# Kernel optimization log

Hardware: AMD Instinct MI355X
Metric: run time of the kernel (lower is better)

## Reference

```python
import jax, jax.numpy as jnp
import numpy as np

NUM_LEVELS = 8
CODEBOOK_SIZE = 1024
D_MODEL = 512


def setup_inputs() -> dict:
    key = jax.random.key(0)
    kx, kc = jax.random.split(key)
    x = jax.random.normal(kx, (8, 4096, D_MODEL), dtype=jnp.float32)
    # stacked embedding tables, one per RVQ level: [L, K, D]
    codebooks = jax.random.normal(kc, (NUM_LEVELS, CODEBOOK_SIZE, D_MODEL), dtype=jnp.float32)
    return {"x": x, "codebooks": codebooks}


def reference(x, codebooks):
    """Residual VQ: per level, nearest-codebook lookup on the residual.

    x: [B, N, D], codebooks: [L, K, D].
    Returns (quantized [B, N, D] with straight-through estimator, indices [B, N, L]).
    """
    residual = x
    q_sum = jnp.zeros_like(x)
    all_indices = []
    for l in range(codebooks.shape[0]):
        cb = codebooks[l]  # [K, D]
        # squared Euclidean distance; argmin matches torch.cdist argmin
        r2 = jnp.sum(residual * residual, axis=-1, keepdims=True)      # [B, N, 1]
        c2 = jnp.sum(cb * cb, axis=-1)                                  # [K]
        cross = jnp.einsum("bnd,kd->bnk", residual, cb)                # [B, N, K]
        dist2 = r2 - 2.0 * cross + c2                                   # [B, N, K]
        idx = jnp.argmin(dist2, axis=-1)                                # [B, N]
        all_indices.append(idx)
        q = cb[idx]                                                     # gather: [B, N, D]
        q_sum = q_sum + q
        residual = residual - q
    # straight-through: forward value is q_sum, gradient flows to x only
    quantized = x + jax.lax.stop_gradient(q_sum - x)
    return quantized, jnp.stack(all_indices, axis=-1)
```

## Files before the change

kernel.cpp:

```cpp
#include <hip/hip_runtime.h>
#include <stdint.h>

#define NLV 8
#define KCB 1024
#define DM  512
#define NTOK (8*4096)
#define BETA 0.00390625f

typedef _Float16 f16;
typedef f16  f16x4 __attribute__((ext_vector_type(4)));
typedef f16  f16x8 __attribute__((ext_vector_type(8)));
typedef float f32x4 __attribute__((ext_vector_type(4)));

typedef __attribute__((address_space(1))) const unsigned int* as1p;
typedef __attribute__((address_space(3))) unsigned int*       as3p;
__device__ __forceinline__ void gll16(const void* g, void* l) {
    __builtin_amdgcn_global_load_lds((as1p)g, (as3p)l, 16, 0, 0);
}

__global__ void c2_kernel(const float* __restrict__ cbs, float* __restrict__ c2) {
    int row  = blockIdx.x;
    int lane = threadIdx.x;
    const float4* p4 = (const float4*)(cbs + (size_t)row * DM);
    float4 a = p4[lane];
    float4 b = p4[lane + 64];
    float s = a.x*a.x + a.y*a.y + a.z*a.z + a.w*a.w
            + b.x*b.x + b.y*b.y + b.z*b.z + b.w*b.w;
    float t = (float)(f16)a.x + (float)(f16)a.y + (float)(f16)a.z + (float)(f16)a.w
            + (float)(f16)b.x + (float)(f16)b.y + (float)(f16)b.z + (float)(f16)b.w;
    #pragma unroll
    for (int off = 32; off > 0; off >>= 1) {
        s += __shfl_down(s, off, 64);
        t += __shfl_down(t, off, 64);
    }
    if (lane == 0) c2[row] = s + 2.0f * BETA * t;
}

__global__ void split_kernel(const float* __restrict__ src,
                             f16* __restrict__ hi, f16* __restrict__ lo) {
    size_t i = (size_t)blockIdx.x * 256 + threadIdx.x;
    float4 v = ((const float4*)src)[i];
    f16x4 h, l;
    h.x = (f16)v.x; l.x = (f16)((v.x - (float)h.x) + BETA);
    h.y = (f16)v.y; l.y = (f16)((v.y - (float)h.y) + BETA);
    h.z = (f16)v.z; l.z = (f16)((v.z - (float)h.z) + BETA);
    h.w = (f16)v.w; l.w = (f16)((v.w - (float)h.w) + BETA);
    ((f16x4*)hi)[i] = h;
    ((f16x4*)lo)[i] = l;
}

#define MBT  64
#define NCH  256
#define KS   32
#define NTHR 256
#define BUFB 40960

__global__ __launch_bounds__(NTHR, 2)
void rvq_mfma(const float* __restrict__ xin, float* __restrict__ qout,
              const float* __restrict__ cbs,
              const f16* __restrict__ Bhi, const f16* __restrict__ Blo,
              f16* __restrict__ Ahi, f16* __restrict__ Alo,
              const float* __restrict__ c2g, float* __restrict__ idxout,
              int lvl, int is_last)
{
    __shared__ char smem[2 * BUFB];
    const int tid  = threadIdx.x;
    const int lane = tid & 63;
    const int wn   = tid >> 6;
    const int tx   = lane & 15;
    const int q    = lane >> 4;
    const size_t tok0 = (size_t)blockIdx.x * MBT;

    const f16*   Bh_l = Bhi + (size_t)lvl * KCB * DM;
    const f16*   Bl_l = Blo + (size_t)lvl * KCB * DM;
    const float* c2l  = c2g + lvl * KCB;
    const float* cbl  = cbs + (size_t)lvl * KCB * DM;

    const int srow = tid >> 2;
    const int sg   = (tid & 3) ^ ((srow >> 1) & 3);
    const int rsw  = q ^ ((tx >> 1) & 3);

    auto stage = [&](char* buf, int cb0, int k0) {
        const int ko = k0 + sg * 8;
        char* wb = buf + wn * 1024;
        const size_t ga = (tok0 + srow) * (size_t)DM + ko;
        gll16(&Ahi[ga], wb);
        gll16(&Alo[ga], wb + 4096);
        #pragma unroll
        for (int i = 0; i < 4; ++i) {
            const size_t gb = (size_t)(cb0 + 64 * i + srow) * DM + ko;
            gll16(&Bh_l[gb], wb +  8192 + 4096 * i);
            gll16(&Bl_l[gb], wb + 24576 + 4096 * i);
        }
    };

    int aoff[4], boff[4];
    #pragma unroll
    for (int i = 0; i < 4; ++i) aoff[i] = (i * 16 + tx) * 64 + rsw * 16;
    #pragma unroll
    for (int j = 0; j < 4; ++j) boff[j] = (wn * 64 + j * 16 + tx) * 64 + rsw * 16;

    float bestv[16];
    int   besti[16];
    #pragma unroll
    for (int t = 0; t < 16; ++t) { bestv[t] = 3.4e38f; besti[t] = 0; }

    stage(smem, 0, 0);

    for (int ch = 0; ch < KCB / NCH; ++ch) {
        f32x4 acc[4][4];
        #pragma unroll
        for (int i = 0; i < 4; ++i)
            #pragma unroll
            for (int j = 0; j < 4; ++j) acc[i][j] = (f32x4)0.0f;

        for (int kk = 0; kk < 16; ++kk) {
            const int gk = ch * 16 + kk;
            char* bb = smem + (gk & 1) * BUFB;
            char* bn = smem + ((gk & 1) ^ 1) * BUFB;
            __syncthreads();
            if (gk + 1 < 64)
                stage(bn, ((gk + 1) >> 4) * NCH, ((gk + 1) & 15) * KS);

            f16x8 ah[4], al[4], bh[4], bl[4];
            #pragma unroll
            for (int i = 0; i < 4; ++i) {
                ah[i] = *(const f16x8*)(bb +        aoff[i]);
                al[i] = *(const f16x8*)(bb + 4096 + aoff[i]);
            }
            #pragma unroll
            for (int j = 0; j < 4; ++j) {
                bh[j] = *(const f16x8*)(bb +  8192 + boff[j]);
                bl[j] = *(const f16x8*)(bb + 24576 + boff[j]);
            }
            #pragma unroll
            for (int j = 0; j < 4; ++j)
                #pragma unroll
                for (int i = 0; i < 4; ++i)
                    acc[i][j] = __builtin_amdgcn_mfma_f32_16x16x32_f16(ah[i], bh[j], acc[i][j], 0, 0, 0);
            #pragma unroll
            for (int j = 0; j < 4; ++j)
                #pragma unroll
                for (int i = 0; i < 4; ++i)
                    acc[i][j] = __builtin_amdgcn_mfma_f32_16x16x32_f16(ah[i], bl[j], acc[i][j], 0, 0, 0);
            #pragma unroll
            for (int j = 0; j < 4; ++j)
                #pragma unroll
                for (int i = 0; i < 4; ++i)
                    acc[i][j] = __builtin_amdgcn_mfma_f32_16x16x32_f16(al[i], bh[j], acc[i][j], 0, 0, 0);
        }

        const int cb0 = ch * NCH;
        #pragma unroll
        for (int j = 0; j < 4; ++j) {
            int n = cb0 + wn * 64 + j * 16 + tx;
            float c2v = c2l[n];
            #pragma unroll
            for (int i = 0; i < 4; ++i)
                #pragma unroll
                for (int r = 0; r < 4; ++r) {
                    float s = fmaf(-2.f, acc[i][j][r], c2v);
                    int t = i * 4 + r;
                    if (s < bestv[t]) { bestv[t] = s; besti[t] = n; }
                }
        }
    }

    #pragma unroll
    for (int t = 0; t < 16; ++t) {
        float v = bestv[t]; int bi = besti[t];
        #pragma unroll
        for (int off = 1; off < 16; off <<= 1) {
            float ov = __shfl_xor(v, off, 64);
            int   oi = __shfl_xor(bi, off, 64);
            if (ov < v || (ov == v && oi < bi)) { v = ov; bi = oi; }
        }
        bestv[t] = v; besti[t] = bi;
    }

    float* redV = (float*)smem;
    int*   redI = (int*)(smem + 1024);
    int*   kbst = (int*)(smem + 2048);
    __syncthreads();
    if (tx == 0) {
        #pragma unroll
        for (int i = 0; i < 4; ++i)
            #pragma unroll
            for (int r = 0; r < 4; ++r) {
                int m = i * 16 + q * 4 + r;
                redV[wn * 64 + m] = bestv[i * 4 + r];
                redI[wn * 64 + m] = besti[i * 4 + r];
            }
    }
    __syncthreads();
    if (tid < MBT) {
        float bv = redV[tid]; int bi = redI[tid];
        #pragma unroll
        for (int w = 1; w < 4; ++w) {
            float v  = redV[w * 64 + tid];
            int   ii = redI[w * 64 + tid];
            if (v < bv || (v == bv && ii < bi)) { bv = v; bi = ii; }
        }
        kbst[tid] = bi;
        idxout[(tok0 + tid) * NLV + lvl] = (float)bi;
    }
    __syncthreads();

    #pragma unroll 4
    for (int it = 0; it < 16; ++it) {
        int e  = it * NTHR + tid;
        int t  = e >> 6, d8 = e & 63;
        size_t go = (tok0 + t) * (size_t)DM + d8 * 8;
        f16x8 h8 = *(const f16x8*)&Ahi[go];
        f16x8 l8 = *(const f16x8*)&Alo[go];
        const float* cp = &cbl[(size_t)kbst[t] * DM + d8 * 8];
        float4 c0 = *(const float4*)cp;
        float4 c1 = *(const float4*)(cp + 4);
        float r[8];
        r[0] = (float)h8[0] + ((float)l8[0] - BETA) - c0.x;
        r[1] = (float)h8[1] + ((float)l8[1] - BETA) - c0.y;
        r[2] = (float)h8[2] + ((float)l8[2] - BETA) - c0.z;
        r[3] = (float)h8[3] + ((float)l8[3] - BETA) - c0.w;
        r[4] = (float)h8[4] + ((float)l8[4] - BETA) - c1.x;
        r[5] = (float)h8[5] + ((float)l8[5] - BETA) - c1.y;
        r[6] = (float)h8[6] + ((float)l8[6] - BETA) - c1.z;
        r[7] = (float)h8[7] + ((float)l8[7] - BETA) - c1.w;
        if (is_last) {
            float4 x0 = *(const float4*)&xin[go];
            float4 x1 = *(const float4*)&xin[go + 4];
            float4 q0 = make_float4(x0.x - r[0], x0.y - r[1], x0.z - r[2], x0.w - r[3]);
            float4 q1 = make_float4(x1.x - r[4], x1.y - r[5], x1.z - r[6], x1.w - r[7]);
            *(float4*)&qout[go]     = q0;
            *(float4*)&qout[go + 4] = q1;
        } else {
            f16x8 h, l;
            #pragma unroll
            for (int k = 0; k < 8; ++k) {
                h[k] = (f16)r[k];
                l[k] = (f16)((r[k] - (float)h[k]) + BETA);
            }
            *(f16x8*)&Ahi[go] = h;
            *(f16x8*)&Alo[go] = l;
        }
    }
}

extern "C" void kernel_launch(void* const* d_in, const int* in_sizes, int n_in,
                              void* d_out, int out_size, void* d_ws, size_t ws_size,
                              hipStream_t stream) {
    const float* x   = (const float*)d_in[0];
    const float* cbs = (const float*)d_in[1];
    float* qout   = (float*)d_out;
    float* idxout = qout + (size_t)NTOK * DM;

    const size_t B_ELE = (size_t)NLV * KCB * DM;
    const size_t A_ELE = (size_t)NTOK * DM;

    f16* Bhi = (f16*)d_ws;
    f16* Blo = Bhi + B_ELE;
    f16* Ahi = Blo + B_ELE;
    f16* Alo = Ahi + A_ELE;
    float* c2 = (float*)(Alo + A_ELE);

    split_kernel<<<(int)(B_ELE / 4 / 256), 256, 0, stream>>>(cbs, Bhi, Blo);
    split_kernel<<<(int)(A_ELE / 4 / 256), 256, 0, stream>>>(x, Ahi, Alo);
    c2_kernel<<<NLV * KCB, 64, 0, stream>>>(cbs, c2);

    const int nblocks = NTOK / MBT;
    for (int l = 0; l < NLV; ++l) {
        rvq_mfma<<<nblocks, NTHR, 0, stream>>>(x, qout, cbs,
                                               Bhi, Blo, Ahi, Alo, c2, idxout,
                                               l, (l == NLV - 1) ? 1 : 0);
    }
}
```

Before: 1.131 ms.

## Load MFMA operands directly from global memory instead of LDS staging

Removes the double-buffered LDS staging (global_load_lds) and per-step barriers in the distance GEMM loop, and reads each wave's A/B fp16 hi/lo fragments directly from global memory. LDS shrinks to the small reduction buffers. This avoids barrier and staging overhead but makes every wave fetch A fragments redundantly through the caches, and removes explicit prefetch overlap, so load latency may be exposed.

```diff
diff --git a/kernel.cpp b/kernel.cpp
--- a/kernel.cpp
+++ b/kernel.cpp
@@ -11,12 +11,6 @@
 typedef f16  f16x4 __attribute__((ext_vector_type(4)));
 typedef f16  f16x8 __attribute__((ext_vector_type(8)));
 typedef float f32x4 __attribute__((ext_vector_type(4)));
-
-typedef __attribute__((address_space(1))) const unsigned int* as1p;
-typedef __attribute__((address_space(3))) unsigned int*       as3p;
-__device__ __forceinline__ void gll16(const void* g, void* l) {
-    __builtin_amdgcn_global_load_lds((as1p)g, (as3p)l, 16, 0, 0);
-}
 
 __global__ void c2_kernel(const float* __restrict__ cbs, float* __restrict__ c2) {
     int row  = blockIdx.x;
@@ -51,9 +45,7 @@
 
 #define MBT  64
 #define NCH  256
-#define KS   32
 #define NTHR 256
-#define BUFB 40960
 
 __global__ __launch_bounds__(NTHR, 2)
 void rvq_mfma(const float* __restrict__ xin, float* __restrict__ qout,
@@ -63,7 +55,10 @@
               const float* __restrict__ c2g, float* __restrict__ idxout,
               int lvl, int is_last)
 {
-    __shared__ char smem[2 * BUFB];
+    __shared__ float redV[4 * MBT];
+    __shared__ int   redI[4 * MBT];
+    __shared__ int   kbst[MBT];
+
     const int tid  = threadIdx.x;
     const int lane = tid & 63;
     const int wn   = tid >> 6;
@@ -71,68 +66,51 @@
     const int q    = lane >> 4;
     const size_t tok0 = (size_t)blockIdx.x * MBT;
 
-    const f16*   Bh_l = Bhi + (size_t)lvl * KCB * DM;
-    const f16*   Bl_l = Blo + (size_t)lvl * KCB * DM;
-    const float* c2l  = c2g + lvl * KCB;
-    const float* cbl  = cbs + (size_t)lvl * KCB * DM;
-
-    const int srow = tid >> 2;
-    const int sg   = (tid & 3) ^ ((srow >> 1) & 3);
-    const int rsw  = q ^ ((tx >> 1) & 3);
-
-    auto stage = [&](char* buf, int cb0, int k0) {
-        const int ko = k0 + sg * 8;
-        char* wb = buf + wn * 1024;
-        const size_t ga = (tok0 + srow) * (size_t)DM + ko;
-        gll16(&Ahi[ga], wb);
-        gll16(&Alo[ga], wb + 4096);
-        #pragma unroll
-        for (int i = 0; i < 4; ++i) {
-            const size_t gb = (size_t)(cb0 + 64 * i + srow) * DM + ko;
-            gll16(&Bh_l[gb], wb +  8192 + 4096 * i);
-            gll16(&Bl_l[gb], wb + 24576 + 4096 * i);
-        }
-    };
-
-    int aoff[4], boff[4];
-    #pragma unroll
-    for (int i = 0; i < 4; ++i) aoff[i] = (i * 16 + tx) * 64 + rsw * 16;
-    #pragma unroll
-    for (int j = 0; j < 4; ++j) boff[j] = (wn * 64 + j * 16 + tx) * 64 + rsw * 16;
+    const f16* __restrict__ Bh_l = Bhi + (size_t)lvl * KCB * DM;
+    const f16* __restrict__ Bl_l = Blo + (size_t)lvl * KCB * DM;
+    const float* __restrict__ c2l = c2g + lvl * KCB;
+    const float* __restrict__ cbl = cbs + (size_t)lvl * KCB * DM;
+
+    size_t abase[4];
+    #pragma unroll
+    for (int i = 0; i < 4; ++i)
+        abase[i] = (tok0 + (size_t)(i * 16 + tx)) * DM + q * 8;
 
     float bestv[16];
     int   besti[16];
     #pragma unroll
     for (int t = 0; t < 16; ++t) { bestv[t] = 3.4e38f; besti[t] = 0; }
 
-    stage(smem, 0, 0);
-
     for (int ch = 0; ch < KCB / NCH; ++ch) {
+        const int cb0 = ch * NCH;
+
+        size_t bbase[4];
+        #pragma unroll
+        for (int j = 0; j < 4; ++j)
+            bbase[j] = ((size_t)(cb0 + wn * 64 + j * 16 + tx)) * DM + q * 8;
+
         f32x4 acc[4][4];
         #pragma unroll
         for (int i = 0; i < 4; ++i)
             #pragma unroll
             for (int j = 0; j < 4; ++j) acc[i][j] = (f32x4)0.0f;
 
-        for (int kk = 0; kk < 16; ++kk) {
-            const int gk = ch * 16 + kk;
-            char* bb = smem + (gk & 1) * BUFB;
-            char* bn = smem + ((gk & 1) ^ 1) * BUFB;
-            __syncthreads();
-            if (gk + 1 < 64)
-                stage(bn, ((gk + 1) >> 4) * NCH, ((gk + 1) & 15) * KS);
+        #pragma unroll 4
+        for (int ks = 0; ks < 16; ++ks) {
+            const int ko = ks * 32;
 
             f16x8 ah[4], al[4], bh[4], bl[4];
             #pragma unroll
             for (int i = 0; i < 4; ++i) {
-                ah[i] = *(const f16x8*)(bb +        aoff[i]);
-                al[i] = *(const f16x8*)(bb + 4096 + aoff[i]);
+                ah[i] = *(const f16x8*)(Ahi + abase[i] + ko);
+                al[i] = *(const f16x8*)(Alo + abase[i] + ko);
             }
             #pragma unroll
             for (int j = 0; j < 4; ++j) {
-                bh[j] = *(const f16x8*)(bb +  8192 + boff[j]);
-                bl[j] = *(const f16x8*)(bb + 24576 + boff[j]);
-            }
+                bh[j] = *(const f16x8*)(Bh_l + bbase[j] + ko);
+                bl[j] = *(const f16x8*)(Bl_l + bbase[j] + ko);
+            }
+
             #pragma unroll
             for (int j = 0; j < 4; ++j)
                 #pragma unroll
@@ -150,7 +128,6 @@
                     acc[i][j] = __builtin_amdgcn_mfma_f32_16x16x32_f16(al[i], bh[j], acc[i][j], 0, 0, 0);
         }
 
-        const int cb0 = ch * NCH;
         #pragma unroll
         for (int j = 0; j < 4; ++j) {
             int n = cb0 + wn * 64 + j * 16 + tx;
@@ -178,10 +155,6 @@
         bestv[t] = v; besti[t] = bi;
     }
 
-    float* redV = (float*)smem;
-    int*   redI = (int*)(smem + 1024);
-    int*   kbst = (int*)(smem + 2048);
-    __syncthreads();
     if (tx == 0) {
         #pragma unroll
         for (int i = 0; i < 4; ++i)
```

Result: slower. 2.113 ms (+86.8%).

## Split operand staging into phases interleaved with MFMA groups and partial waits

Applied to the files above, without the earlier changes.

The single per-step stage-all-then-syncthreads pattern is replaced by three staged loads: A, then B-hi, then B-lo. Each is issued between MFMA groups and separated by raw s_barriers, with an explicit vmcnt wait instead of a full drain. MFMA sections are wrapped in s_setprio so compute waves get priority while the next tile streams in. The aim is to overlap global-to-LDS traffic with matrix math and cut full-barrier stalls. In exchange, stageA writes the next buffer before any barrier while slower waves may still be reading A-lo from that buffer, which risks a race. It also issues harmless extra loads on the final step.

```diff
diff --git a/kernel.cpp b/kernel.cpp
--- a/kernel.cpp
+++ b/kernel.cpp
@@ -17,6 +17,8 @@
 __device__ __forceinline__ void gll16(const void* g, void* l) {
     __builtin_amdgcn_global_load_lds((as1p)g, (as3p)l, 16, 0, 0);
 }
+
+#define VMCNT(n) asm volatile("s_waitcnt vmcnt(" #n ")" ::: "memory")
 
 __global__ void c2_kernel(const float* __restrict__ cbs, float* __restrict__ c2) {
     int row  = blockIdx.x;
@@ -80,18 +82,28 @@
     const int sg   = (tid & 3) ^ ((srow >> 1) & 3);
     const int rsw  = q ^ ((tx >> 1) & 3);
 
-    auto stage = [&](char* buf, int cb0, int k0) {
-        const int ko = k0 + sg * 8;
+    auto stageA = [&](char* buf, int gk2) {
+        const int ko = (gk2 & 15) * KS + sg * 8;
         char* wb = buf + wn * 1024;
         const size_t ga = (tok0 + srow) * (size_t)DM + ko;
         gll16(&Ahi[ga], wb);
         gll16(&Alo[ga], wb + 4096);
-        #pragma unroll
-        for (int i = 0; i < 4; ++i) {
-            const size_t gb = (size_t)(cb0 + 64 * i + srow) * DM + ko;
-            gll16(&Bh_l[gb], wb +  8192 + 4096 * i);
-            gll16(&Bl_l[gb], wb + 24576 + 4096 * i);
-        }
+    };
+    auto stageBh = [&](char* buf, int gk2) {
+        const int cb0 = (gk2 >> 4) * NCH;
+        const int ko  = (gk2 & 15) * KS + sg * 8;
+        char* wb = buf + wn * 1024;
+        #pragma unroll
+        for (int i = 0; i < 4; ++i)
+            gll16(&Bh_l[(size_t)(cb0 + 64 * i + srow) * DM + ko], wb + 8192 + 4096 * i);
+    };
+    auto stageBl = [&](char* buf, int gk2) {
+        const int cb0 = (gk2 >> 4) * NCH;
+        const int ko  = (gk2 & 15) * KS + sg * 8;
+        char* wb = buf + wn * 1024;
+        #pragma unroll
+        for (int i = 0; i < 4; ++i)
+            gll16(&Bl_l[(size_t)(cb0 + 64 * i + srow) * DM + ko], wb + 24576 + 4096 * i);
     };
 
     int aoff[4], boff[4];
@@ -105,7 +117,7 @@
     #pragma unroll
     for (int t = 0; t < 16; ++t) { bestv[t] = 3.4e38f; besti[t] = 0; }
 
-    stage(smem, 0, 0);
+    stageA(smem, 0); stageBh(smem, 0); stageBl(smem, 0);
 
     for (int ch = 0; ch < KCB / NCH; ++ch) {
         f32x4 acc[4][4];
@@ -116,38 +128,57 @@
 
         for (int kk = 0; kk < 16; ++kk) {
             const int gk = ch * 16 + kk;
+            const int nx = (gk + 1) & 63;
             char* bb = smem + (gk & 1) * BUFB;
             char* bn = smem + ((gk & 1) ^ 1) * BUFB;
-            __syncthreads();
-            if (gk + 1 < 64)
-                stage(bn, ((gk + 1) >> 4) * NCH, ((gk + 1) & 15) * KS);
+
+            stageA(bn, nx);
+            __builtin_amdgcn_sched_barrier(0);
+            VMCNT(2);
+            __builtin_amdgcn_s_barrier();
+            __builtin_amdgcn_sched_barrier(0);
 
             f16x8 ah[4], al[4], bh[4], bl[4];
             #pragma unroll
-            for (int i = 0; i < 4; ++i) {
-                ah[i] = *(const f16x8*)(bb +        aoff[i]);
-                al[i] = *(const f16x8*)(bb + 4096 + aoff[i]);
-            }
-            #pragma unroll
-            for (int j = 0; j < 4; ++j) {
-                bh[j] = *(const f16x8*)(bb +  8192 + boff[j]);
-                bl[j] = *(const f16x8*)(bb + 24576 + boff[j]);
-            }
+            for (int i = 0; i < 4; ++i) ah[i] = *(const f16x8*)(bb + aoff[i]);
+            #pragma unroll
+            for (int j = 0; j < 4; ++j) bh[j] = *(const f16x8*)(bb + 8192 + boff[j]);
+
+            __builtin_amdgcn_s_setprio(1);
             #pragma unroll
             for (int j = 0; j < 4; ++j)
                 #pragma unroll
                 for (int i = 0; i < 4; ++i)
                     acc[i][j] = __builtin_amdgcn_mfma_f32_16x16x32_f16(ah[i], bh[j], acc[i][j], 0, 0, 0);
+            __builtin_amdgcn_s_setprio(0);
+
+            stageBh(bn, nx);
+            __builtin_amdgcn_s_barrier();
+
+            #pragma unroll
+            for (int j = 0; j < 4; ++j) bl[j] = *(const f16x8*)(bb + 24576 + boff[j]);
+
+            __builtin_amdgcn_s_setprio(1);
             #pragma unroll
             for (int j = 0; j < 4; ++j)
                 #pragma unroll
                 for (int i = 0; i < 4; ++i)
                     acc[i][j] = __builtin_amdgcn_mfma_f32_16x16x32_f16(ah[i], bl[j], acc[i][j], 0, 0, 0);
+            __builtin_amdgcn_s_setprio(0);
+
+            stageBl(bn, nx);
+            __builtin_amdgcn_s_barrier();
+
+            #pragma unroll
+            for (int i = 0; i < 4; ++i) al[i] = *(const f16x8*)(bb + 4096 + aoff[i]);
+
+            __builtin_amdgcn_s_setprio(1);
             #pragma unroll
             for (int j = 0; j < 4; ++j)
                 #pragma unroll
                 for (int i = 0; i < 4; ++i)
                     acc[i][j] = __builtin_amdgcn_mfma_f32_16x16x32_f16(al[i], bh[j], acc[i][j], 0, 0, 0);
+            __builtin_amdgcn_s_setprio(0);
         }
 
         const int cb0 = ch * NCH;
```

After: 1.147 ms. No clear change (+1.3%).

## Split block tile across 8 waves with per-wave staging and MFMA priority

Applied to the files above, without the earlier changes.

Doubles threads per block to 512 and splits the 64-token tile across two wave rows, so each wave computes a 32x64 sub-tile with half the accumulators. The global-to-LDS staging is reassigned: lower waves load hi halves and upper waves load lo halves, so each thread issues fewer loads. It also raises launch-bounds occupancy to 4 and wraps the MFMA sequence in s_setprio. The goal is more waves in flight to hide latency, at the cost of duplicated B-fragment LDS reads per wave pair and higher register pressure under the new bounds.

```diff
diff --git a/kernel.cpp b/kernel.cpp
--- a/kernel.cpp
+++ b/kernel.cpp
@@ -52,10 +52,10 @@
 #define MBT  64
 #define NCH  256
 #define KS   32
-#define NTHR 256
+#define NTHR 512
 #define BUFB 40960
 
-__global__ __launch_bounds__(NTHR, 2)
+__global__ __launch_bounds__(NTHR, 4)
 void rvq_mfma(const float* __restrict__ xin, float* __restrict__ qout,
               const float* __restrict__ cbs,
               const f16* __restrict__ Bhi, const f16* __restrict__ Blo,
@@ -66,7 +66,9 @@
     __shared__ char smem[2 * BUFB];
     const int tid  = threadIdx.x;
     const int lane = tid & 63;
-    const int wn   = tid >> 6;
+    const int w    = tid >> 6;
+    const int wn   = w & 3;
+    const int wm   = w >> 2;
     const int tx   = lane & 15;
     const int q    = lane >> 4;
     const size_t tok0 = (size_t)blockIdx.x * MBT;
@@ -76,41 +78,47 @@
     const float* c2l  = c2g + lvl * KCB;
     const float* cbl  = cbs + (size_t)lvl * KCB * DM;
 
-    const int srow = tid >> 2;
-    const int sg   = (tid & 3) ^ ((srow >> 1) & 3);
+    const int rloc = lane >> 2;
+    const int sg   = (lane & 3) ^ ((lane >> 3) & 3);
     const int rsw  = q ^ ((tx >> 1) & 3);
 
-    auto stage = [&](char* buf, int cb0, int k0) {
-        const int ko = k0 + sg * 8;
-        char* wb = buf + wn * 1024;
-        const size_t ga = (tok0 + srow) * (size_t)DM + ko;
-        gll16(&Ahi[ga], wb);
-        gll16(&Alo[ga], wb + 4096);
-        #pragma unroll
-        for (int i = 0; i < 4; ++i) {
-            const size_t gb = (size_t)(cb0 + 64 * i + srow) * DM + ko;
-            gll16(&Bh_l[gb], wb +  8192 + 4096 * i);
-            gll16(&Bl_l[gb], wb + 24576 + 4096 * i);
-        }
+    const int arow = (w & 3) * 16 + rloc;
+    const f16* pA  = (w < 4 ? Ahi : Alo) + (tok0 + arow) * (size_t)DM + sg * 8;
+    const int aLds = (w < 4 ? 0 : 4096) + (w & 3) * 1024;
+
+    const f16* pB = (w < 4 ? Bh_l : Bl_l);
+    int bElo[4];
+    #pragma unroll
+    for (int i = 0; i < 4; ++i)
+        bElo[i] = (((w & 3) * 4 + i) * 16 + rloc) * DM + sg * 8;
+
+    auto stage = [&](char* buf, int gk2) {
+        const int ko  = (gk2 & 15) * KS;
+        const int cb0 = (gk2 >> 4) * NCH;
+        gll16(pA + ko, buf + aLds);
+        const size_t bo = (size_t)cb0 * DM + ko;
+        #pragma unroll
+        for (int i = 0; i < 4; ++i)
+            gll16(pB + bo + bElo[i], buf + 8192 + (w * 4 + i) * 1024);
     };
 
-    int aoff[4], boff[4];
-    #pragma unroll
-    for (int i = 0; i < 4; ++i) aoff[i] = (i * 16 + tx) * 64 + rsw * 16;
+    int aoff[2], boff[4];
+    #pragma unroll
+    for (int i = 0; i < 2; ++i) aoff[i] = (wm * 32 + i * 16 + tx) * 64 + rsw * 16;
     #pragma unroll
     for (int j = 0; j < 4; ++j) boff[j] = (wn * 64 + j * 16 + tx) * 64 + rsw * 16;
 
-    float bestv[16];
-    int   besti[16];
-    #pragma unroll
-    for (int t = 0; t < 16; ++t) { bestv[t] = 3.4e38f; besti[t] = 0; }
-
-    stage(smem, 0, 0);
+    float bestv[8];
+    int   besti[8];
+    #pragma unroll
+    for (int t = 0; t < 8; ++t) { bestv[t] = 3.4e38f; besti[t] = 0; }
+
+    stage(smem, 0);
 
     for (int ch = 0; ch < KCB / NCH; ++ch) {
-        f32x4 acc[4][4];
-        #pragma unroll
-        for (int i = 0; i < 4; ++i)
+        f32x4 acc[2][4];
+        #pragma unroll
+        for (int i = 0; i < 2; ++i)
             #pragma unroll
             for (int j = 0; j < 4; ++j) acc[i][j] = (f32x4)0.0f;
 
@@ -118,36 +126,40 @@
             const int gk = ch * 16 + kk;
             char* bb = smem + (gk & 1) * BUFB;
             char* bn = smem + ((gk & 1) ^ 1) * BUFB;
+
             __syncthreads();
             if (gk + 1 < 64)
-                stage(bn, ((gk + 1) >> 4) * NCH, ((gk + 1) & 15) * KS);
-
-            f16x8 ah[4], al[4], bh[4], bl[4];
-            #pragma unroll
-            for (int i = 0; i < 4; ++i) {
-                ah[i] = *(const f16x8*)(bb +        aoff[i]);
+                stage(bn, gk + 1);
+
+            f16x8 ah[2], al[2], bh[4], bl[4];
+            #pragma unroll
+            for (int i = 0; i < 2; ++i) {
+                ah[i] = *(const f16x8*)(bb + aoff[i]);
                 al[i] = *(const f16x8*)(bb + 4096 + aoff[i]);
             }
             #pragma unroll
             for (int j = 0; j < 4; ++j) {
-                bh[j] = *(const f16x8*)(bb +  8192 + boff[j]);
+                bh[j] = *(const f16x8*)(bb + 8192 + boff[j]);
                 bl[j] = *(const f16x8*)(bb + 24576 + boff[j]);
             }
+
+            __builtin_amdgcn_s_setprio(1);
             #pragma unroll
             for (int j = 0; j < 4; ++j)
                 #pragma unroll
-                for (int i = 0; i < 4; ++i)
+                for (int i = 0; i < 2; ++i)
                     acc[i][j] = __builtin_amdgcn_mfma_f32_16x16x32_f16(ah[i], bh[j], acc[i][j], 0, 0, 0);
             #pragma unroll
             for (int j = 0; j < 4; ++j)
                 #pragma unroll
-                for (int i = 0; i < 4; ++i)
+                for (int i = 0; i < 2; ++i)
                     acc[i][j] = __builtin_amdgcn_mfma_f32_16x16x32_f16(ah[i], bl[j], acc[i][j], 0, 0, 0);
             #pragma unroll
             for (int j = 0; j < 4; ++j)
                 #pragma unroll
-                for (int i = 0; i < 4; ++i)
+                for (int i = 0; i < 2; ++i)
                     acc[i][j] = __builtin_amdgcn_mfma_f32_16x16x32_f16(al[i], bh[j], acc[i][j], 0, 0, 0);
+            __builtin_amdgcn_s_setprio(0);
         }
 
         const int cb0 = ch * NCH;
@@ -156,7 +168,7 @@
             int n = cb0 + wn * 64 + j * 16 + tx;
             float c2v = c2l[n];
             #pragma unroll
-            for (int i = 0; i < 4; ++i)
+            for (int i = 0; i < 2; ++i)
                 #pragma unroll
                 for (int r = 0; r < 4; ++r) {
                     float s = fmaf(-2.f, acc[i][j][r], c2v);
@@ -167,7 +179,7 @@
     }
 
     #pragma unroll
-    for (int t = 0; t < 16; ++t) {
+    for (int t = 0; t < 8; ++t) {
         float v = bestv[t]; int bi = besti[t];
         #pragma unroll
         for (int off = 1; off < 16; off <<= 1) {
@@ -184,10 +196,10 @@
     __syncthreads();
     if (tx == 0) {
         #pragma unroll
-        for (int i = 0; i < 4; ++i)
+        for (int i = 0; i < 2; ++i)
             #pragma unroll
             for (int r = 0; r < 4; ++r) {
-                int m = i * 16 + q * 4 + r;
+                int m = wm * 32 + i * 16 + q * 4 + r;
                 redV[wn * 64 + m] = bestv[i * 4 + r];
                 redI[wn * 64 + m] = besti[i * 4 + r];
             }
@@ -196,9 +208,9 @@
     if (tid < MBT) {
         float bv = redV[tid]; int bi = redI[tid];
         #pragma unroll
-        for (int w = 1; w < 4; ++w) {
-            float v  = redV[w * 64 + tid];
-            int   ii = redI[w * 64 + tid];
+        for (int ww = 1; ww < 4; ++ww) {
+            float v  = redV[ww * 64 + tid];
+            int   ii = redI[ww * 64 + tid];
             if (v < bv || (v == bv && ii < bi)) { bv = v; bi = ii; }
         }
         kbst[tid] = bi;
@@ -207,7 +219,7 @@
     __syncthreads();
 
     #pragma unroll 4
-    for (int it = 0; it < 16; ++it) {
+    for (int it = 0; it < 8; ++it) {
         int e  = it * NTHR + tid;
         int t  = e >> 6, d8 = e & 63;
         size_t go = (tok0 + t) * (size_t)DM + d8 * 8;
```

After: 1.270 ms. 1.12x slower.
